# Kernel optimization log

Hardware: AMD Instinct MI355X
Metric: run time of the kernel (lower is better)

## Reference

```python
import jax, jax.numpy as jnp
import numpy as np

N_NODES = 50000
N_EDGES = 1600000
N_FEAT = 128
HIDDEN = 128
N_GRAPHS = 64
N_CLASSES = 10
N_REGS = 1


def setup_inputs() -> dict:
    key = jax.random.key(0)
    ks = jax.random.split(key, 16)
    inp = {
        "x": jax.random.normal(ks[0], (N_NODES, N_FEAT), dtype=jnp.float32),
        "edge_index": jax.random.randint(ks[1], (2, N_EDGES), 0, N_NODES, dtype=jnp.int32),
        "batch": jnp.sort(jax.random.randint(ks[2], (N_NODES,), 0, N_GRAPHS, dtype=jnp.int32)),
        # GCNConv layer params (PyG: linear without bias applied first, bias added after aggregation)
        "w0": jax.random.normal(ks[3], (N_FEAT, HIDDEN), dtype=jnp.float32) * 0.05,
        "b0": jax.random.normal(ks[4], (HIDDEN,), dtype=jnp.float32) * 0.05,
        "w1": jax.random.normal(ks[5], (HIDDEN, HIDDEN), dtype=jnp.float32) * 0.05,
        "b1": jax.random.normal(ks[6], (HIDDEN,), dtype=jnp.float32) * 0.05,
        "w2": jax.random.normal(ks[7], (HIDDEN, HIDDEN), dtype=jnp.float32) * 0.05,
        "b2": jax.random.normal(ks[8], (HIDDEN,), dtype=jnp.float32) * 0.05,
        # heads
        "wc": jax.random.normal(ks[9], (HIDDEN, N_CLASSES), dtype=jnp.float32) * 0.05,
        "bc": jax.random.normal(ks[10], (N_CLASSES,), dtype=jnp.float32) * 0.05,
        "wr": jax.random.normal(ks[11], (HIDDEN, N_REGS), dtype=jnp.float32) * 0.05,
        "br": jax.random.normal(ks[12], (N_REGS,), dtype=jnp.float32) * 0.05,
    }
    return inp


def _gcn_layer(x, src, dst, w, b, deg_inv_sqrt, deg_inv):
    # x: [N, Din] -> [N, Dout]. GCNConv: D^-1/2 (A+I) D^-1/2 (x W) + b
    h = x @ w  # [N, Dout]
    coef = (deg_inv_sqrt[src] * deg_inv_sqrt[dst])[:, None]  # [E, 1]
    agg = jax.ops.segment_sum(h[src] * coef, dst, num_segments=x.shape[0])
    agg = agg + h * deg_inv[:, None]  # self-loop term: deg^-1 * h
    return agg + b


def reference(x, edge_index, batch, w0, b0, w1, b1, w2, b2, wc, bc, wr, br):
    src, dst = edge_index[0], edge_index[1]
    n = x.shape[0]
    # degrees include self-loop weight 1 (PyG gcn_norm with edge_weight=1)
    deg = jax.ops.segment_sum(jnp.ones(src.shape, x.dtype), dst, num_segments=n) + 1.0
    deg_inv_sqrt = deg ** -0.5
    deg_inv = 1.0 / deg

    h = _gcn_layer(x, src, dst, w0, b0, deg_inv_sqrt, deg_inv)
    h = _gcn_layer(jax.nn.elu(h), src, dst, w1, b1, deg_inv_sqrt, deg_inv)
    h = _gcn_layer(jax.nn.elu(h), src, dst, w2, b2, deg_inv_sqrt, deg_inv)

    # global mean pool over graphs
    sums = jax.ops.segment_sum(h, batch, num_segments=N_GRAPHS)  # [G, H]
    cnt = jax.ops.segment_sum(jnp.ones((n,), h.dtype), batch, num_segments=N_GRAPHS)
    pooled = sums / jnp.maximum(cnt, 1.0)[:, None]

    cls_out = pooled @ wc + bc
    reg_out = pooled @ wr + br
    return (pooled, cls_out, reg_out)
```

## Files before the change

### kernel.cpp

```cpp
#include <hip/hip_runtime.h>
#include <hip/hip_fp16.h>
#include <math.h>

#define N_NODES   50000
#define N_EDGES   1600000
#define NF        128
#define N_GRAPHS  64
#define N_CLASSES 10

#define NBK       391
#define BK_SHIFT  7
#define BK_NODES  128
#define SLAB      5120
#define CHUNK     4096
#define NCHUNKS   ((N_EDGES + CHUNK - 1) / CHUNK)
#define NODES_PER_BLK 8
#define NBLK_AGG  (N_NODES / NODES_PER_BLK)
#define TILE_SHIFT 13
#define NTILE     8

typedef _Float16 half8 __attribute__((ext_vector_type(8)));
typedef float f32x4 __attribute__((ext_vector_type(4)));

__global__ void k_init(int* __restrict__ bucket_cur, float* __restrict__ sums,
                       const float* __restrict__ w0, const float* __restrict__ w1,
                       const float* __restrict__ w2, _Float16* __restrict__ wf) {
    int b = blockIdx.x, t = threadIdx.x;
    if (b < 3) {
        const float* W = (b == 0) ? w0 : (b == 1) ? w1 : w2;
        _Float16* dst = wf + (size_t)b * NF * NF;
        for (int idx = t; idx < NF * NF; idx += 256) {
            int k = idx >> 7, n = idx & 127;
            int nt = n >> 4, kc = k >> 5, quad = (k >> 3) & 3, j = k & 7;
            int lane = quad * 16 + (n & 15);
            dst[((nt * 4 + kc) * 64 + lane) * 8 + j] = (_Float16)W[idx];
        }
    } else {
        int i = (b - 3) * 256 + t;
        if (i < NBK) bucket_cur[i] = i * SLAB;
        if (i < N_GRAPHS * NF) sums[i] = 0.f;
    }
}

__global__ __launch_bounds__(256) void k_bscatter(const int* __restrict__ src,
                                                  const int* __restrict__ dst,
                                                  int* __restrict__ bucket_cur,
                                                  int* __restrict__ pairs) {
    __shared__ int h[NBK], rb[NBK], c2[NBK];
    int t = threadIdx.x;
    for (int i = t; i < NBK; i += 256) { h[i] = 0; c2[i] = 0; }
    __syncthreads();
    int base = blockIdx.x * CHUNK;
    int end = min(base + CHUNK, N_EDGES);
    for (int e = base + t; e < end; e += 256)
        atomicAdd(&h[dst[e] >> BK_SHIFT], 1);
    __syncthreads();
    for (int i = t; i < NBK; i += 256)
        rb[i] = h[i] ? atomicAdd(&bucket_cur[i], h[i]) : 0;
    __syncthreads();
    for (int e = base + t; e < end; e += 256) {
        int d = dst[e];
        int b = d >> BK_SHIFT;
        int k = atomicAdd(&c2[b], 1);
        pairs[rb[b] + k] = (src[e] << BK_SHIFT) | (d & (BK_NODES - 1));
    }
}

__global__ __launch_bounds__(512) void k_bfill(const int* __restrict__ pairs,
                                               const int* __restrict__ bucket_cur,
                                               int* __restrict__ row_start,
                                               int* __restrict__ row_end,
                                               float* __restrict__ dis,
                                               int* __restrict__ csr_src) {
    __shared__ int cnt[BK_NODES * NTILE];
    __shared__ int cur[BK_NODES * NTILE];
    __shared__ int pos[BK_NODES * NTILE + 1];
    __shared__ int ts[512];
    int b = blockIdx.x, t = threadIdx.x;
    int node_base = b << BK_SHIFT;
    int lo = b * SLAB, hi = bucket_cur[b];

    cnt[t] = 0; cnt[t + 512] = 0;
    __syncthreads();
    for (int e = lo + t; e < hi; e += 512) {
        int p = pairs[e];
        atomicAdd(&cnt[(p & (BK_NODES - 1)) * NTILE + (p >> (BK_SHIFT + TILE_SHIFT))], 1);
    }
    __syncthreads();

    int a0 = cnt[2 * t], a1 = cnt[2 * t + 1];
    ts[t] = a0 + a1;
    __syncthreads();
    for (int off = 1; off < 512; off <<= 1) {
        int y = (t >= off) ? ts[t - off] : 0;
        __syncthreads();
        ts[t] += y;
        __syncthreads();
    }
    int ex = lo + ts[t] - (a0 + a1);
    pos[2 * t] = ex;       cur[2 * t] = ex;
    pos[2 * t + 1] = ex + a0; cur[2 * t + 1] = ex + a0;
    if (t == 511) pos[1024] = lo + ts[511];
    __syncthreads();

    if (t < BK_NODES) {
        int n = node_base + t;
        if (n < N_NODES) {
            int r0 = pos[t * NTILE], r1 = pos[(t + 1) * NTILE];
            row_start[n] = r0;
            row_end[n]   = r1;
            dis[n] = rsqrtf((float)(r1 - r0 + 1));
        }
    }
    __syncthreads();

    for (int e = lo + t; e < hi; e += 512) {
        int p = pairs[e];
        int idx = (p & (BK_NODES - 1)) * NTILE + (p >> (BK_SHIFT + TILE_SHIFT));
        int ps = atomicAdd(&cur[idx], 1);
        csr_src[ps] = p >> BK_SHIFT;
    }
}

template <bool ELU, bool FP32IN>
__global__ __launch_bounds__(256) void k_gemm(const void* __restrict__ Xv,
                                              const _Float16* __restrict__ WF,
                                              const float* __restrict__ dis,
                                              __half* __restrict__ H) {
    __shared__ _Float16 xs[64 * 136];
    const _Float16* Xh = (const _Float16*)Xv;
    const float*    Xf = (const float*)Xv;
    int t = threadIdx.x;
    int row0 = blockIdx.x * 64;
#pragma unroll
    for (int i = 0; i < 4; i++) {
        int f = i * 256 + t;
        int r = f >> 4, c = (f & 15) * 8;
        int gr = row0 + r;
        half8 v = {};
        if (gr < N_NODES) {
            if (FP32IN) {
                float4 v0 = *(const float4*)&Xf[(size_t)gr * NF + c];
                float4 v1 = *(const float4*)&Xf[(size_t)gr * NF + c + 4];
                v[0] = (_Float16)v0.x; v[1] = (_Float16)v0.y;
                v[2] = (_Float16)v0.z; v[3] = (_Float16)v0.w;
                v[4] = (_Float16)v1.x; v[5] = (_Float16)v1.y;
                v[6] = (_Float16)v1.z; v[7] = (_Float16)v1.w;
            } else {
                v = *(const half8*)&Xh[(size_t)gr * NF + c];
            }
        }
        if (ELU) {
#pragma unroll
            for (int j = 0; j < 8; j++) {
                float xv = (float)v[j];
                v[j] = (_Float16)(xv > 0.f ? xv : (expf(xv) - 1.f));
            }
        }
        *(half8*)&xs[r * 136 + c] = v;
    }
    __syncthreads();

    int w = t >> 6;
    int lane = t & 63;
    int m = lane & 15, quad = lane >> 4;

    half8 a[4];
#pragma unroll
    for (int kc = 0; kc < 4; kc++)
        a[kc] = *(const half8*)&xs[(w * 16 + m) * 136 + kc * 32 + quad * 8];

    f32x4 acc[8];
#pragma unroll
    for (int nt = 0; nt < 8; nt++) {
        f32x4 c4 = {0.f, 0.f, 0.f, 0.f};
#pragma unroll
        for (int kc = 0; kc < 4; kc++) {
            half8 bf = *(const half8*)&WF[((nt * 4 + kc) * 64 + lane) * 8];
            c4 = __builtin_amdgcn_mfma_f32_16x16x32_f16(a[kc], bf, c4, 0, 0, 0);
        }
        acc[nt] = c4;
    }

    __syncthreads();
#pragma unroll
    for (int reg = 0; reg < 4; reg++) {
        int r = w * 16 + quad * 4 + reg;
        int gr = row0 + r;
        float ds = (gr < N_NODES) ? dis[gr] : 0.f;
#pragma unroll
        for (int nt = 0; nt < 8; nt++)
            xs[r * 136 + nt * 16 + m] = (_Float16)(ds * acc[nt][reg]);
    }
    __syncthreads();
#pragma unroll
    for (int i = 0; i < 4; i++) {
        int f = i * 256 + t;
        int r = f >> 4, c = (f & 15) * 8;
        int gr = row0 + r;
        if (gr < N_NODES)
            *(half8*)&H[(size_t)gr * NF + c] = *(const half8*)&xs[r * 136 + c];
    }
}

__global__ __launch_bounds__(256) void k_agg(const __half* __restrict__ H,
                                             const float* __restrict__ bias,
                                             const int* __restrict__ row_start,
                                             const int* __restrict__ row_end,
                                             const int* __restrict__ csr_src,
                                             const float* __restrict__ dis,
                                             __half* __restrict__ outh) {
    const uint2* H4 = (const uint2*)H;
    int t = threadIdx.x;
    int lane = t & 63;
    int node = blockIdx.x * NODES_PER_BLK + (t >> 6) * 2 + (lane >> 5);
    int l    = lane & 31;
    if (node >= N_NODES) return;
    int rs = row_start[node], re = row_end[node];
    float a0 = 0.f, a1 = 0.f, a2 = 0.f, a3 = 0.f;
    int e = rs;
    for (; e + 7 < re; e += 8) {
        uint2 v[8];
#pragma unroll
        for (int j = 0; j < 8; j++) {
            int s = csr_src[e + j];
            v[j] = H4[(size_t)s * 32 + l];
        }
#pragma unroll
        for (int j = 0; j < 8; j++) {
            float2 lo = __half22float2(*(__half2*)&v[j].x);
            float2 hi = __half22float2(*(__half2*)&v[j].y);
            a0 += lo.x; a1 += lo.y; a2 += hi.x; a3 += hi.y;
        }
    }
    for (; e < re; e++) {
        int s = csr_src[e];
        uint2 v = H4[(size_t)s * 32 + l];
        float2 lo = __half22float2(*(__half2*)&v.x);
        float2 hi = __half22float2(*(__half2*)&v.y);
        a0 += lo.x; a1 += lo.y; a2 += hi.x; a3 += hi.y;
    }
    {
        uint2 v = H4[(size_t)node * 32 + l];
        float2 lo = __half22float2(*(__half2*)&v.x);
        float2 hi = __half22float2(*(__half2*)&v.y);
        a0 += lo.x; a1 += lo.y; a2 += hi.x; a3 += hi.y;
    }
    float di = dis[node];
    int c = l * 4;
    float4 bv = *(const float4*)&bias[c];
    uint2 o;
    *(__half2*)&o.x = __floats2half2_rn(a0 * di + bv.x, a1 * di + bv.y);
    *(__half2*)&o.y = __floats2half2_rn(a2 * di + bv.z, a3 * di + bv.w);
    ((uint2*)outh)[(size_t)node * 32 + l] = o;
}

__global__ void k_pool(const __half* __restrict__ A, const int* __restrict__ batch,
                       float* __restrict__ sums) {
    int b = blockIdx.x, t = threadIdx.x;
    int c = t & 127, th = t >> 7;
    int start = b * 256 + th;
    if (start >= N_NODES) return;
    int end = min(N_NODES, b * 256 + 256);
    float acc = 0.f;
    int gcur = batch[start];
    for (int i = start; i < end; i += 2) {
        int g = batch[i];
        if (g != gcur) {
            atomicAdd(&sums[gcur * NF + c], acc);
            acc = 0.f;
            gcur = g;
        }
        acc += __half2float(A[(size_t)i * NF + c]);
    }
    atomicAdd(&sums[gcur * NF + c], acc);
}

__global__ void k_head(const float* __restrict__ sums, const int* __restrict__ batch,
                       const float* __restrict__ wc, const float* __restrict__ bc,
                       const float* __restrict__ wr, const float* __restrict__ br,
                       float* __restrict__ out) {
    __shared__ float p[128];
    __shared__ int sh[2];
    int g = blockIdx.x, c = threadIdx.x;
    if (c < 2) {
        int tgt = g + c;
        int lo = 0, hi = N_NODES;
        while (lo < hi) { int m = (lo + hi) >> 1; if (batch[m] < tgt) lo = m + 1; else hi = m; }
        sh[c] = lo;
    }
    __syncthreads();
    int s0 = sh[0], s1 = sh[1];
    float cnt = (float)max(s1 - s0, 1);
    float pv = sums[g * NF + c] / cnt;
    p[c] = pv;
    out[g * NF + c] = pv;
    __syncthreads();
    if (c < N_CLASSES) {
        float d = bc[c];
        for (int k = 0; k < NF; k++) d += p[k] * wc[k * N_CLASSES + c];
        out[N_GRAPHS * NF + g * N_CLASSES + c] = d;
    }
    if (c == N_CLASSES) {
        float d = br[0];
        for (int k = 0; k < NF; k++) d += p[k] * wr[k];
        out[N_GRAPHS * NF + N_GRAPHS * N_CLASSES + g] = d;
    }
}

extern "C" void kernel_launch(void* const* d_in, const int* in_sizes, int n_in,
                              void* d_out, int out_size, void* d_ws, size_t ws_size,
                              hipStream_t stream) {
    const float* x     = (const float*)d_in[0];
    const int*   ei    = (const int*)d_in[1];
    const int*   batch = (const int*)d_in[2];
    const float* w0 = (const float*)d_in[3];
    const float* b0 = (const float*)d_in[4];
    const float* w1 = (const float*)d_in[5];
    const float* b1 = (const float*)d_in[6];
    const float* w2 = (const float*)d_in[7];
    const float* b2 = (const float*)d_in[8];
    const float* wc = (const float*)d_in[9];
    const float* bc = (const float*)d_in[10];
    const float* wr = (const float*)d_in[11];
    const float* br = (const float*)d_in[12];
    const int* srcp = ei;
    const int* dstp = ei + N_EDGES;
    float* out = (float*)d_out;

    char* ws = (char*)d_ws;
    size_t off = 0;
    auto alloc = [&](size_t bytes) -> void* {
        void* p = ws + off;
        off = (off + bytes + 255) & ~(size_t)255;
        return p;
    };
    int*      row_start  = (int*)alloc(N_NODES * 4);
    int*      row_end    = (int*)alloc(N_NODES * 4);
    int*      bucket_cur = (int*)alloc(NBK * 4);
    float*    dis        = (float*)alloc(N_NODES * 4);
    int*      csr_src    = (int*)alloc((size_t)NBK * SLAB * 4);
    __half*   Hbuf       = (__half*)alloc((size_t)N_NODES * NF * 2);
    _Float16* Ah         = (_Float16*)alloc((size_t)N_NODES * NF * 2);
    _Float16* wf         = (_Float16*)alloc((size_t)3 * NF * NF * 2);
    float*    sums       = (float*)alloc(N_GRAPHS * NF * 4);
    (void)ws_size;
    int* pairs = (int*)Hbuf;

    k_init<<<35, 256, 0, stream>>>(bucket_cur, sums, w0, w1, w2, wf);
    k_bscatter<<<NCHUNKS, 256, 0, stream>>>(srcp, dstp, bucket_cur, pairs);
    k_bfill<<<NBK, 512, 0, stream>>>(pairs, bucket_cur, row_start, row_end, dis, csr_src);

    const int gemm_grid = (N_NODES + 63) / 64;

    k_gemm<false, true><<<gemm_grid, 256, 0, stream>>>(x, wf, dis, Hbuf);
    k_agg<<<NBLK_AGG, 256, 0, stream>>>(Hbuf, b0, row_start, row_end, csr_src, dis, (__half*)Ah);
    k_gemm<true, false><<<gemm_grid, 256, 0, stream>>>(Ah, wf + NF * NF, dis, Hbuf);
    k_agg<<<NBLK_AGG, 256, 0, stream>>>(Hbuf, b1, row_start, row_end, csr_src, dis, (__half*)Ah);
    k_gemm<true, false><<<gemm_grid, 256, 0, stream>>>(Ah, wf + 2 * NF * NF, dis, Hbuf);
    k_agg<<<NBLK_AGG, 256, 0, stream>>>(Hbuf, b2, row_start, row_end, csr_src, dis, (__half*)Ah);

    k_pool<<<(N_NODES + 255) / 256, 256, 0, stream>>>((__half*)Ah, batch, sums);
    k_head<<<N_GRAPHS, 128, 0, stream>>>(sums, batch, wc, bc, wr, br, out);
}
```

Baseline: 390.1 us.

## Use nontemporal loads/stores, register-cache edges in scatter, shuffle CSR indices in aggregation

The bucket scatter now loads each edge's src and dst once into registers, keeps the packed pair and bucket id there, and writes from registers in the second pass instead of rereading global memory. Nontemporal loads and stores are added to the streaming accesses in scatter, fill, aggregation output and pooling so they disturb the cache less. The aggregation kernel loads 8 CSR indices with one per-lane load and broadcasts them through wave shuffles instead of having every lane load each index. The pool kernel processes two halves per thread across 4 row groups. The risks are higher register pressure from the per-thread arrays and the possibility that nontemporal stores evict data, such as the layer output, that the next kernel would have read from cache.

After: 446.3 us. 1.14x slower.

```diff
diff --git a/kernel.cpp b/kernel.cpp
--- a/kernel.cpp
+++ b/kernel.cpp
@@ -14,6 +14,7 @@
 #define SLAB      5120
 #define CHUNK     4096
 #define NCHUNKS   ((N_EDGES + CHUNK - 1) / CHUNK)
+#define EPT       (CHUNK / 256)
 #define NODES_PER_BLK 8
 #define NBLK_AGG  (N_NODES / NODES_PER_BLK)
 #define TILE_SHIFT 13
@@ -51,18 +52,31 @@
     for (int i = t; i < NBK; i += 256) { h[i] = 0; c2[i] = 0; }
     __syncthreads();
     int base = blockIdx.x * CHUNK;
-    int end = min(base + CHUNK, N_EDGES);
-    for (int e = base + t; e < end; e += 256)
-        atomicAdd(&h[dst[e] >> BK_SHIFT], 1);
+    int pk[EPT];
+    int bk[EPT];
+#pragma unroll
+    for (int k = 0; k < EPT; k++) {
+        int e = base + t + k * 256;
+        if (e < N_EDGES) {
+            int d = __builtin_nontemporal_load(&dst[e]);
+            int s = __builtin_nontemporal_load(&src[e]);
+            bk[k] = d >> BK_SHIFT;
+            pk[k] = (s << BK_SHIFT) | (d & (BK_NODES - 1));
+            atomicAdd(&h[bk[k]], 1);
+        } else {
+            bk[k] = -1;
+        }
+    }
     __syncthreads();
     for (int i = t; i < NBK; i += 256)
         rb[i] = h[i] ? atomicAdd(&bucket_cur[i], h[i]) : 0;
     __syncthreads();
-    for (int e = base + t; e < end; e += 256) {
-        int d = dst[e];
-        int b = d >> BK_SHIFT;
-        int k = atomicAdd(&c2[b], 1);
-        pairs[rb[b] + k] = (src[e] << BK_SHIFT) | (d & (BK_NODES - 1));
+#pragma unroll
+    for (int k = 0; k < EPT; k++) {
+        if (bk[k] >= 0) {
+            int p = atomicAdd(&c2[bk[k]], 1);
+            __builtin_nontemporal_store(pk[k], &pairs[rb[bk[k]] + p]);
+        }
     }
 }
 
@@ -118,7 +132,7 @@
         int p = pairs[e];
         int idx = (p & (BK_NODES - 1)) * NTILE + (p >> (BK_SHIFT + TILE_SHIFT));
         int ps = atomicAdd(&cur[idx], 1);
-        csr_src[ps] = p >> BK_SHIFT;
+        __builtin_nontemporal_store(p >> BK_SHIFT, &csr_src[ps]);
     }
 }
 
@@ -215,15 +229,17 @@
     int lane = t & 63;
     int node = blockIdx.x * NODES_PER_BLK + (t >> 6) * 2 + (lane >> 5);
     int l    = lane & 31;
+    int halfbase = lane & 32;
     if (node >= N_NODES) return;
     int rs = row_start[node], re = row_end[node];
     float a0 = 0.f, a1 = 0.f, a2 = 0.f, a3 = 0.f;
     int e = rs;
     for (; e + 7 < re; e += 8) {
+        int myidx = __builtin_nontemporal_load(&csr_src[e + (l & 7)]);
         uint2 v[8];
 #pragma unroll
         for (int j = 0; j < 8; j++) {
-            int s = csr_src[e + j];
+            int s = __shfl(myidx, halfbase + j, 64);
             v[j] = H4[(size_t)s * 32 + l];
         }
 #pragma unroll
@@ -234,7 +250,7 @@
         }
     }
     for (; e < re; e++) {
-        int s = csr_src[e];
+        int s = __builtin_nontemporal_load(&csr_src[e]);
         uint2 v = H4[(size_t)s * 32 + l];
         float2 lo = __half22float2(*(__half2*)&v.x);
         float2 hi = __half22float2(*(__half2*)&v.y);
@@ -252,28 +268,34 @@
     uint2 o;
     *(__half2*)&o.x = __floats2half2_rn(a0 * di + bv.x, a1 * di + bv.y);
     *(__half2*)&o.y = __floats2half2_rn(a2 * di + bv.z, a3 * di + bv.w);
-    ((uint2*)outh)[(size_t)node * 32 + l] = o;
+    __builtin_nontemporal_store(*(unsigned long long*)&o,
+        (unsigned long long*)&((uint2*)outh)[(size_t)node * 32 + l]);
 }
 
 __global__ void k_pool(const __half* __restrict__ A, const int* __restrict__ batch,
                        float* __restrict__ sums) {
+    const unsigned int* A2 = (const unsigned int*)A;
     int b = blockIdx.x, t = threadIdx.x;
-    int c = t & 127, th = t >> 7;
-    int start = b * 256 + th;
+    int grp = t >> 6, l = t & 63;
+    int start = b * 256 + grp;
     if (start >= N_NODES) return;
     int end = min(N_NODES, b * 256 + 256);
-    float acc = 0.f;
+    float ax = 0.f, ay = 0.f;
     int gcur = batch[start];
-    for (int i = start; i < end; i += 2) {
+    for (int i = start; i < end; i += 4) {
         int g = batch[i];
         if (g != gcur) {
-            atomicAdd(&sums[gcur * NF + c], acc);
-            acc = 0.f;
+            atomicAdd(&sums[gcur * NF + 2 * l], ax);
+            atomicAdd(&sums[gcur * NF + 2 * l + 1], ay);
+            ax = 0.f; ay = 0.f;
             gcur = g;
         }
-        acc += __half2float(A[(size_t)i * NF + c]);
-    }
-    atomicAdd(&sums[gcur * NF + c], acc);
+        unsigned int u = __builtin_nontemporal_load(&A2[(size_t)i * 64 + l]);
+        float2 f = __half22float2(*(__half2*)&u);
+        ax += f.x; ay += f.y;
+    }
+    atomicAdd(&sums[gcur * NF + 2 * l], ax);
+    atomicAdd(&sums[gcur * NF + 2 * l + 1], ay);
 }
 
 __global__ void k_head(const float* __restrict__ sums, const int* __restrict__ batch,
```
